# Kernel tuning notes

Hardware: AMD Instinct MI355X
Metric: run time of the kernel (lower is better)

Reference implementation:

```python
import jax, jax.numpy as jnp
import numpy as np
from jax import lax

H = 512      # hidden_dim
P = 11       # num_patches
T = 200      # patch_size
STRIDE = 180 # patch_stride
L = 2000     # output_length
C = 8        # num_target_channels
B = 1024


def _conv1d(x, w, b, pad):
    # x: (B, Cin, L), w: (Cout, Cin, K) torch OIH layout
    y = lax.conv_general_dilated(x, w, window_strides=(1,), padding=[(pad, pad)],
                                 dimension_numbers=('NCH', 'OIH', 'NCH'))
    return y + b[None, :, None]


def _window():
    fade = min(T // 4, 50)
    w = jnp.ones((T,), dtype=jnp.float32)
    ramp = jnp.linspace(0.0, 1.0, fade, dtype=jnp.float32)
    w = w.at[:fade].set(ramp)
    w = w.at[T - fade:].set(ramp[::-1])
    return w


def setup_inputs() -> dict:
    key = jax.random.key(0)
    ks = jax.random.split(key, 16)
    s = 0.02
    return {
        'expanded_embeddings': jax.random.normal(ks[0], (B, P, C, H), dtype=jnp.float32),
        # patch_decoder: Linear(H,H) -> GELU -> (Dropout eval=identity) -> Linear(H,T)
        'W1': jax.random.normal(ks[1], (H, H), dtype=jnp.float32) * s,
        'b1': jnp.zeros((H,), dtype=jnp.float32),
        'W2': jax.random.normal(ks[2], (H, T), dtype=jnp.float32) * s,
        'b2': jnp.zeros((T,), dtype=jnp.float32),
        # refinement: Conv1d(C,4C,15,p7) GELU Conv1d(4C,2C,15,p7) GELU Conv1d(2C,C,15,p7)
        'rw1': jax.random.normal(ks[3], (4 * C, C, 15), dtype=jnp.float32) * s,
        'rb1': jnp.zeros((4 * C,), dtype=jnp.float32),
        'rw2': jax.random.normal(ks[4], (2 * C, 4 * C, 15), dtype=jnp.float32) * s,
        'rb2': jnp.zeros((2 * C,), dtype=jnp.float32),
        'rw3': jax.random.normal(ks[5], (C, 2 * C, 15), dtype=jnp.float32) * s,
        'rb3': jnp.zeros((C,), dtype=jnp.float32),
        # output_proj: Conv1d(C,C,1)
        'pw': jax.random.normal(ks[6], (C, C, 1), dtype=jnp.float32) * s,
        'pb': jnp.zeros((C,), dtype=jnp.float32),
    }


def reference(expanded_embeddings, W1, b1, W2, b2, rw1, rb1, rw2, rb2, rw3, rb3, pw, pb):
    gelu = lambda x: jax.nn.gelu(x, approximate=False)  # torch default GELU (erf)
    # per-patch MLP decode: (B,P,C,H) -> (B,P,C,T)
    h = gelu(jnp.einsum('bpch,hd->bpcd', expanded_embeddings, W1) + b1)
    patches = jnp.einsum('bpch,ht->bpct', h, W2) + b2

    # overlap-add with triangular-faded window
    win = _window()  # (T,)
    out = jnp.zeros((B, C, L), dtype=jnp.float32)
    wsum = jnp.zeros((L,), dtype=jnp.float32)  # identical across B,C
    for i in range(P):  # small static loop over patches
        s0 = i * STRIDE
        if s0 + T <= L:
            out = out.at[:, :, s0:s0 + T].add(patches[:, i] * win)
            wsum = wsum.at[s0:s0 + T].add(win)
    rec = out / jnp.clip(wsum, 1e-8)[None, None, :]

    # conv refinement + residual
    r = gelu(_conv1d(rec, rw1, rb1, 7))
    r = gelu(_conv1d(r, rw2, rb2, 7))
    r = _conv1d(r, rw3, rb3, 7)
    rec = rec + r
    return _conv1d(rec, pw, pb, 0)
```

## Files before the change

### kernel.cpp

```cpp
#include <hip/hip_runtime.h>
#include <stdint.h>
#include <stddef.h>

#define HD 512
#define NP 11
#define PT 200
#define PSTRIDE 180
#define OL 2000
#define NC 8
#define NB 1024

typedef __bf16 bf16x8 __attribute__((ext_vector_type(8)));
typedef float floatx4 __attribute__((ext_vector_type(4)));
typedef unsigned short ushort8v __attribute__((ext_vector_type(8)));

__device__ __forceinline__ unsigned short f2bf(float f) {
    return __builtin_bit_cast(unsigned short, (__bf16)f);
}
__device__ __forceinline__ float bf2f(unsigned short s) {
    return __uint_as_float(((unsigned int)s) << 16);
}
__device__ __forceinline__ float gelu_erf(float x) {
    float z  = x * 0.70710678118654752440f;
    float az = __builtin_fabsf(z);
    float t  = __builtin_amdgcn_rcpf(__builtin_fmaf(0.3275911f, az, 1.0f));
    float p  = __builtin_fmaf(1.061405429f, t, -1.453152027f);
    p = __builtin_fmaf(p, t, 1.421413741f);
    p = __builtin_fmaf(p, t, -0.284496736f);
    p = __builtin_fmaf(p, t, 0.254829592f);
    p = p * t;
    float e    = __expf(-az * az);
    float erfa = __builtin_fmaf(-p, e, 1.0f);
    float erfz = (z < 0.0f) ? -erfa : erfa;
    return 0.5f * x * (1.0f + erfz);
}
__device__ __forceinline__ void async16(const unsigned short* g, unsigned short* l) {
    __builtin_amdgcn_global_load_lds(
        (const __attribute__((address_space(1))) unsigned int*)g,
        (__attribute__((address_space(3))) unsigned int*)l, 16, 0, 0);
}

__global__ __launch_bounds__(256) void prep_w_kernel(const float* __restrict__ W1,
                                                     const float* __restrict__ W2,
                                                     unsigned short* __restrict__ W1t,
                                                     unsigned short* __restrict__ W2t) {
    int idx = blockIdx.x * 256 + threadIdx.x;
    if (idx < 512 * 512) {
        int n = idx >> 9, k = idx & 511;
        W1t[idx] = f2bf(W1[k * 512 + n]);
    } else {
        int j = idx - 512 * 512;
        int n = j >> 9, k = j & 511;
        W2t[j] = (n < PT) ? f2bf(W2[k * PT + n]) : (unsigned short)0;
    }
}

__global__ __launch_bounds__(256) void prep_cw_kernel(const float* __restrict__ rw1,
                                                      const float* __restrict__ rw2,
                                                      const float* __restrict__ rw3,
                                                      unsigned short* __restrict__ Wt1,
                                                      unsigned short* __restrict__ Wt2,
                                                      unsigned short* __restrict__ Wt3) {
    int idx = blockIdx.x * 256 + threadIdx.x;
    if (idx < 4096) {
        int kb = idx >> 10, rem = idx & 1023, oc = rem >> 5, k = rem & 31;
        int tl = k >> 3, ic = k & 7, tap = kb * 4 + tl;
        Wt1[idx] = (tap < 15) ? f2bf(rw1[(oc * 8 + ic) * 15 + tap]) : (unsigned short)0;
    } else if (idx < 4096 + 7680) {
        int j = idx - 4096;
        int t = j >> 9, rem = j & 511, oc = rem >> 5, ic = rem & 31;
        Wt2[j] = f2bf(rw2[(oc * 32 + ic) * 15 + t]);
    } else {
        int j = idx - 11776;
        int kb = j >> 9, rem = j & 511, m = rem >> 5, k = rem & 31;
        int tl = k >> 4, ic = k & 15, tap = kb * 2 + tl;
        Wt3[j] = (m < 8 && tap < 15) ? f2bf(rw3[(m * 16 + ic) * 15 + tap]) : (unsigned short)0;
    }
}

template<bool A_FP32, bool FUSE_GELU, bool OUT_BF16, int LOG2_NT>
__global__ __launch_bounds__(256) void gemm_lds_kernel(const void* __restrict__ Ain,
                                                       const unsigned short* __restrict__ Bt,
                                                       const float* __restrict__ bias,
                                                       void* __restrict__ Cout,
                                                       int out_stride, int n_valid) {
    __shared__ __align__(16) unsigned short As[128 * 32];
    __shared__ __align__(16) unsigned short Bs[128 * 32];
    const float* Af          = (const float*)Ain;
    const unsigned short* Ab = (const unsigned short*)Ain;
    const int tid  = threadIdx.x;
    const int lane = tid & 63;
    const int wid  = tid >> 6;
    const int bid  = blockIdx.x;
    const int nt   = (bid >> 3) & ((1 << LOG2_NT) - 1);
    const int mt   = (bid >> (3 + LOG2_NT)) * 8 + (bid & 7);
    const int m0 = mt * 128;
    const int n0 = nt * 128;
    const int mw = (wid >> 1) * 64;
    const int nw = (wid & 1) * 64;
    const int l15  = lane & 15;
    const int quad = lane >> 4;
    const int srow = lane >> 2;
    const int scol = (lane & 3) * 8;

    floatx4 acc[4][4];
#pragma unroll
    for (int i = 0; i < 4; ++i)
#pragma unroll
        for (int j = 0; j < 4; ++j) acc[i][j] = (floatx4)0.0f;

    float4 pv[2][2];
    auto loadA = [&](int k0) {
#pragma unroll
        for (int p = 0; p < 2; ++p) {
            const float* g = Af + (size_t)(m0 + wid * 32 + p * 16 + srow) * 512 + k0 + scol;
            pv[p][0] = *(const float4*)g;
            pv[p][1] = *(const float4*)(g + 4);
        }
    };
    if (A_FP32) loadA(0);

    for (int k0 = 0; k0 < 512; k0 += 32) {
#pragma unroll
        for (int p = 0; p < 2; ++p) {
            const int rbase = wid * 32 + p * 16;
            if (A_FP32) {
                ushort8v o;
                o[0] = f2bf(pv[p][0].x); o[1] = f2bf(pv[p][0].y);
                o[2] = f2bf(pv[p][0].z); o[3] = f2bf(pv[p][0].w);
                o[4] = f2bf(pv[p][1].x); o[5] = f2bf(pv[p][1].y);
                o[6] = f2bf(pv[p][1].z); o[7] = f2bf(pv[p][1].w);
                *(ushort8v*)(As + (rbase + srow) * 32 + scol) = o;
            } else {
                async16(Ab + (size_t)(m0 + rbase + srow) * 512 + k0 + scol, As + rbase * 32);
            }
            async16(Bt + (size_t)(n0 + rbase + srow) * 512 + k0 + scol, Bs + rbase * 32);
        }
        __syncthreads();
        if (A_FP32 && k0 + 32 < 512) loadA(k0 + 32);
        bf16x8 af[4], bfr[4];
#pragma unroll
        for (int t = 0; t < 4; ++t) {
            af[t]  = *(const bf16x8*)(As + (mw + t * 16 + l15) * 32 + quad * 8);
            bfr[t] = *(const bf16x8*)(Bs + (nw + t * 16 + l15) * 32 + quad * 8);
        }
#pragma unroll
        for (int mtl = 0; mtl < 4; ++mtl)
#pragma unroll
            for (int ntl = 0; ntl < 4; ++ntl)
                acc[mtl][ntl] = __builtin_amdgcn_mfma_f32_16x16x32_bf16(af[mtl], bfr[ntl], acc[mtl][ntl], 0, 0, 0);
        __syncthreads();
    }

#pragma unroll
    for (int mtl = 0; mtl < 4; ++mtl) {
#pragma unroll
        for (int ntl = 0; ntl < 4; ++ntl) {
            const int col  = n0 + nw + ntl * 16 + l15;
            const int rowb = m0 + mw + mtl * 16 + quad * 4;
            const bool colok = (col < n_valid);
            float bv = colok ? bias[col] : 0.0f;
#pragma unroll
            for (int r = 0; r < 4; ++r) {
                float v = acc[mtl][ntl][r] + bv;
                if (FUSE_GELU) v = gelu_erf(v);
                if (colok) {
                    size_t off = (size_t)(rowb + r) * out_stride + col;
                    if (OUT_BF16) ((unsigned short*)Cout)[off] = f2bf(v);
                    else          ((float*)Cout)[off] = v;
                }
            }
        }
    }
}

__global__ __launch_bounds__(256) void tail_fused(const unsigned short* __restrict__ pat,
                                                  const unsigned short* __restrict__ Wt1,
                                                  const float* __restrict__ rb1,
                                                  const unsigned short* __restrict__ Wt2,
                                                  const float* __restrict__ rb2,
                                                  const unsigned short* __restrict__ Wt3,
                                                  const float* __restrict__ rb3,
                                                  const float* __restrict__ pw,
                                                  const float* __restrict__ pb,
                                                  float* __restrict__ out) {
    __shared__ __align__(16) unsigned short xs[304 * 8];
    __shared__ __align__(16) unsigned short ys1[288 * 40];
    __shared__ __align__(16) unsigned short ys2[272 * 24];
    __shared__ __align__(16) float r2[256 * 12];
    __shared__ float pws[64], bs1[32], bs2[16], bs3[8], bsp[8];
    const int tid = threadIdx.x;
    const int b = blockIdx.y;
    const int seg0 = blockIdx.x * 256;
    const int lane = tid & 63, wid = tid >> 6;
    const int l15 = lane & 15, quad = lane >> 4;

    if (tid < 64) pws[tid] = pw[tid];
    else if (tid < 96)  bs1[tid - 64]  = rb1[tid - 64];
    else if (tid < 112) bs2[tid - 96]  = rb2[tid - 96];
    else if (tid < 120) bs3[tid - 112] = rb3[tid - 112];
    else if (tid < 128) bsp[tid - 120] = pb[tid - 120];

    for (int row = tid; row < 304; row += 256) {
        int p = seg0 - 21 + row;
        float acc[8];
#pragma unroll
        for (int c = 0; c < 8; ++c) acc[c] = 0.0f;
        if (p >= 0 && p < OL) {
            int imin = (p >= PT) ? (p - (PT - PSTRIDE)) / PSTRIDE : 0;
            int imax = p / PSTRIDE; if (imax > NP - 1) imax = NP - 1;
            float wsum = 0.0f;
            for (int i = imin; i <= imax; ++i) {
                int t = p - i * PSTRIDE;
                float w = (t < 50) ? t * (1.0f / 49.0f)
                                   : ((t >= 150) ? (199 - t) * (1.0f / 49.0f) : 1.0f);
                wsum += w;
                const unsigned short* pp = pat + ((size_t)(b * NP + i) * NC) * PT + t;
#pragma unroll
                for (int c = 0; c < 8; ++c) acc[c] += bf2f(pp[c * PT]) * w;
            }
            float inv = 1.0f / fmaxf(wsum, 1e-8f);
#pragma unroll
            for (int c = 0; c < 8; ++c) acc[c] *= inv;
        }
        ushort4 o0, o1;
        o0.x = f2bf(acc[0]); o0.y = f2bf(acc[1]); o0.z = f2bf(acc[2]); o0.w = f2bf(acc[3]);
        o1.x = f2bf(acc[4]); o1.y = f2bf(acc[5]); o1.z = f2bf(acc[6]); o1.w = f2bf(acc[7]);
        *(ushort4*)(xs + row * 8)     = o0;
        *(ushort4*)(xs + row * 8 + 4) = o1;
        int cr = row - 21;
        if (cr >= 0 && cr < 256) {
            float4 v0 = { acc[0], acc[1], acc[2], acc[3] };
            float4 v1 = { acc[4], acc[5], acc[6], acc[7] };
            *(float4*)(r2 + cr * 12)     = v0;
            *(float4*)(r2 + cr * 12 + 4) = v1;
        }
    }
    __syncthreads();

    {
        bf16x8 wf[4][2];
#pragma unroll
        for (int kb = 0; kb < 4; ++kb)
#pragma unroll
            for (int ot = 0; ot < 2; ++ot)
                wf[kb][ot] = *(const bf16x8*)(Wt1 + (kb * 32 + ot * 16 + l15) * 32 + quad * 8);
#pragma unroll
        for (int u = 0; u < 5; ++u) {
            const int base = wid * 80 + u * 16;
            if (base < 288) {
                const int posl = base + l15;
                floatx4 a0 = (floatx4)0.0f, a1 = (floatx4)0.0f;
#pragma unroll
                for (int kb = 0; kb < 4; ++kb) {
                    int row = posl + kb * 4 + quad;
                    bf16x8 bfrag = *(const bf16x8*)(xs + row * 8);
                    a0 = __builtin_amdgcn_mfma_f32_16x16x32_bf16(wf[kb][0], bfrag, a0, 0, 0, 0);
                    a1 = __builtin_amdgcn_mfma_f32_16x16x32_bf16(wf[kb][1], bfrag, a1, 0, 0, 0);
                }
                int oc0 = quad * 4;
                ushort4 o;
                o.x = f2bf(gelu_erf(a0[0] + bs1[oc0]));
                o.y = f2bf(gelu_erf(a0[1] + bs1[oc0 + 1]));
                o.z = f2bf(gelu_erf(a0[2] + bs1[oc0 + 2]));
                o.w = f2bf(gelu_erf(a0[3] + bs1[oc0 + 3]));
                *(ushort4*)(ys1 + posl * 40 + oc0) = o;
                int oc1 = 16 + quad * 4;
                o.x = f2bf(gelu_erf(a1[0] + bs1[oc1]));
                o.y = f2bf(gelu_erf(a1[1] + bs1[oc1 + 1]));
                o.z = f2bf(gelu_erf(a1[2] + bs1[oc1 + 2]));
                o.w = f2bf(gelu_erf(a1[3] + bs1[oc1 + 3]));
                *(ushort4*)(ys1 + posl * 40 + oc1) = o;
            }
        }
    }
    __syncthreads();

    {
        bf16x8 wf[15];
#pragma unroll
        for (int t = 0; t < 15; ++t)
            wf[t] = *(const bf16x8*)(Wt2 + (t * 16 + l15) * 32 + quad * 8);
#pragma unroll
        for (int u = 0; u < 5; ++u) {
            const int base = wid * 80 + u * 16;
            if (base < 272) {
                const int posl = base + l15;
                floatx4 a = (floatx4)0.0f;
#pragma unroll
                for (int t = 0; t < 15; ++t) {
                    bf16x8 bfrag = *(const bf16x8*)(ys1 + (posl + t) * 40 + quad * 8);
                    a = __builtin_amdgcn_mfma_f32_16x16x32_bf16(wf[t], bfrag, a, 0, 0, 0);
                }
                int oc0 = quad * 4;
                ushort4 o;
                o.x = f2bf(gelu_erf(a[0] + bs2[oc0]));
                o.y = f2bf(gelu_erf(a[1] + bs2[oc0 + 1]));
                o.z = f2bf(gelu_erf(a[2] + bs2[oc0 + 2]));
                o.w = f2bf(gelu_erf(a[3] + bs2[oc0 + 3]));
                *(ushort4*)(ys2 + posl * 24 + oc0) = o;
            }
        }
    }
    __syncthreads();

    {
        bf16x8 wf[8];
#pragma unroll
        for (int kb = 0; kb < 8; ++kb)
            wf[kb] = *(const bf16x8*)(Wt3 + (kb * 16 + l15) * 32 + quad * 8);
#pragma unroll
        for (int u = 0; u < 5; ++u) {
            const int base = wid * 80 + u * 16;
            if (base < 256) {
                const int posl = base + l15;
                floatx4 a = (floatx4)0.0f;
#pragma unroll
                for (int kb = 0; kb < 8; ++kb) {
                    int row = posl + kb * 2 + (quad >> 1);
                    bf16x8 bfrag = *(const bf16x8*)(ys2 + row * 24 + (quad & 1) * 8);
                    a = __builtin_amdgcn_mfma_f32_16x16x32_bf16(wf[kb], bfrag, a, 0, 0, 0);
                }
                if (quad < 2) {
                    int oc0 = quad * 4;
                    float4 rv = *(const float4*)(r2 + posl * 12 + oc0);
                    rv.x += a[0] + bs3[oc0];
                    rv.y += a[1] + bs3[oc0 + 1];
                    rv.z += a[2] + bs3[oc0 + 2];
                    rv.w += a[3] + bs3[oc0 + 3];
                    *(float4*)(r2 + posl * 12 + oc0) = rv;
                }
            }
        }
    }
    __syncthreads();

    {
        int p = seg0 + tid;
        if (p < OL) {
            float4 a = *(const float4*)(r2 + tid * 12);
            float4 c = *(const float4*)(r2 + tid * 12 + 4);
#pragma unroll
            for (int o = 0; o < 8; ++o) {
                float v = bsp[o];
                v += pws[o * 8 + 0] * a.x + pws[o * 8 + 1] * a.y + pws[o * 8 + 2] * a.z + pws[o * 8 + 3] * a.w;
                v += pws[o * 8 + 4] * c.x + pws[o * 8 + 5] * c.y + pws[o * 8 + 6] * c.z + pws[o * 8 + 7] * c.w;
                out[((size_t)b * 8 + o) * OL + p] = v;
            }
        }
    }
}

extern "C" void kernel_launch(void* const* d_in, const int* in_sizes, int n_in,
                              void* d_out, int out_size, void* d_ws, size_t ws_size,
                              hipStream_t stream) {
    const float* X   = (const float*)d_in[0];
    const float* W1  = (const float*)d_in[1];
    const float* b1  = (const float*)d_in[2];
    const float* W2  = (const float*)d_in[3];
    const float* b2  = (const float*)d_in[4];
    const float* rw1 = (const float*)d_in[5];
    const float* rb1 = (const float*)d_in[6];
    const float* rw2 = (const float*)d_in[7];
    const float* rb2 = (const float*)d_in[8];
    const float* rw3 = (const float*)d_in[9];
    const float* rb3 = (const float*)d_in[10];
    const float* pw  = (const float*)d_in[11];
    const float* pb  = (const float*)d_in[12];
    float* out = (float*)d_out;

    char* ws = (char*)d_ws;
    unsigned short* W1t = (unsigned short*)(ws +  92274688);
    unsigned short* W2t = (unsigned short*)(ws +  92798976);
    unsigned short* h   = (unsigned short*)(ws +  93061120);
    unsigned short* pat = (unsigned short*)(ws + 185335808);
    unsigned short* Wt1 = (unsigned short*)(ws + 322961408);
    unsigned short* Wt2 = (unsigned short*)(ws + 322969600);
    unsigned short* Wt3 = (unsigned short*)(ws + 322984960);

    prep_w_kernel<<<1536, 256, 0, stream>>>(W1, W2, W1t, W2t);
    prep_cw_kernel<<<62, 256, 0, stream>>>(rw1, rw2, rw3, Wt1, Wt2, Wt3);
    gemm_lds_kernel<true,  true,  true, 2><<<2816, 256, 0, stream>>>((const void*)X, W1t, b1, (void*)h,   512, 512);
    gemm_lds_kernel<false, false, true, 1><<<1408, 256, 0, stream>>>((const void*)h,  W2t, b2, (void*)pat, 200, 200);
    tail_fused<<<dim3(8, NB), 256, 0, stream>>>(pat, Wt1, rb1, Wt2, rb2, Wt3, rb3, pw, pb, out);
}
```

Measured before the change: 548.1 us.

## Load GEMM MFMA fragments directly from global memory instead of staging through LDS

Both GEMM kernels drop the shared-memory tiles and barriers. Each wave now loads its A and B MFMA fragments straight from global memory into registers, with one-step register prefetch of the next k-slice. This removes LDS traffic and __syncthreads stalls. In exchange, tiles are no longer shared across the waves in a block: each A and B row is fetched by two waves, so L2/global traffic doubles and register pressure rises.

```diff
diff --git a/kernel.cpp b/kernel.cpp
--- a/kernel.cpp
+++ b/kernel.cpp
@@ -33,11 +33,6 @@
     float erfa = __builtin_fmaf(-p, e, 1.0f);
     float erfz = (z < 0.0f) ? -erfa : erfa;
     return 0.5f * x * (1.0f + erfz);
-}
-__device__ __forceinline__ void async16(const unsigned short* g, unsigned short* l) {
-    __builtin_amdgcn_global_load_lds(
-        (const __attribute__((address_space(1))) unsigned int*)g,
-        (__attribute__((address_space(3))) unsigned int*)l, 16, 0, 0);
 }
 
 __global__ __launch_bounds__(256) void prep_w_kernel(const float* __restrict__ W1,
@@ -79,13 +74,11 @@
 }
 
 template<bool A_FP32, bool FUSE_GELU, bool OUT_BF16, int LOG2_NT>
-__global__ __launch_bounds__(256) void gemm_lds_kernel(const void* __restrict__ Ain,
-                                                       const unsigned short* __restrict__ Bt,
-                                                       const float* __restrict__ bias,
-                                                       void* __restrict__ Cout,
-                                                       int out_stride, int n_valid) {
-    __shared__ __align__(16) unsigned short As[128 * 32];
-    __shared__ __align__(16) unsigned short Bs[128 * 32];
+__global__ __launch_bounds__(256) void gemm_direct_kernel(const void* __restrict__ Ain,
+                                                          const unsigned short* __restrict__ Bt,
+                                                          const float* __restrict__ bias,
+                                                          void* __restrict__ Cout,
+                                                          int out_stride, int n_valid) {
     const float* Af          = (const float*)Ain;
     const unsigned short* Ab = (const unsigned short*)Ain;
     const int tid  = threadIdx.x;
@@ -100,8 +93,9 @@
     const int nw = (wid & 1) * 64;
     const int l15  = lane & 15;
     const int quad = lane >> 4;
-    const int srow = lane >> 2;
-    const int scol = (lane & 3) * 8;
+
+    const size_t abase = (size_t)(m0 + mw + l15) * 512 + quad * 8;
+    const size_t bbase = (size_t)(n0 + nw + l15) * 512 + quad * 8;
 
     floatx4 acc[4][4];
 #pragma unroll
@@ -109,47 +103,58 @@
 #pragma unroll
         for (int j = 0; j < 4; ++j) acc[i][j] = (floatx4)0.0f;
 
-    float4 pv[2][2];
+    float4 fa[4][2];
+    bf16x8 nA[4];
+    bf16x8 nB[4];
+
+    auto loadB = [&](int k0) {
+#pragma unroll
+        for (int t = 0; t < 4; ++t)
+            nB[t] = *(const bf16x8*)(Bt + bbase + (size_t)t * 16 * 512 + k0);
+    };
     auto loadA = [&](int k0) {
-#pragma unroll
-        for (int p = 0; p < 2; ++p) {
-            const float* g = Af + (size_t)(m0 + wid * 32 + p * 16 + srow) * 512 + k0 + scol;
-            pv[p][0] = *(const float4*)g;
-            pv[p][1] = *(const float4*)(g + 4);
+        if (A_FP32) {
+#pragma unroll
+            for (int t = 0; t < 4; ++t) {
+                const float* g = Af + abase + (size_t)t * 16 * 512 + k0;
+                fa[t][0] = *(const float4*)g;
+                fa[t][1] = *(const float4*)(g + 4);
+            }
+        } else {
+#pragma unroll
+            for (int t = 0; t < 4; ++t)
+                nA[t] = *(const bf16x8*)(Ab + abase + (size_t)t * 16 * 512 + k0);
         }
     };
-    if (A_FP32) loadA(0);
-
-    for (int k0 = 0; k0 < 512; k0 += 32) {
-#pragma unroll
-        for (int p = 0; p < 2; ++p) {
-            const int rbase = wid * 32 + p * 16;
-            if (A_FP32) {
+
+    loadA(0);
+    loadB(0);
+
+    for (int it = 0; it < 16; ++it) {
+        const int kn = it * 32 + 32;
+        bf16x8 af[4], bfr[4];
+        if (A_FP32) {
+#pragma unroll
+            for (int t = 0; t < 4; ++t) {
                 ushort8v o;
-                o[0] = f2bf(pv[p][0].x); o[1] = f2bf(pv[p][0].y);
-                o[2] = f2bf(pv[p][0].z); o[3] = f2bf(pv[p][0].w);
-                o[4] = f2bf(pv[p][1].x); o[5] = f2bf(pv[p][1].y);
-                o[6] = f2bf(pv[p][1].z); o[7] = f2bf(pv[p][1].w);
-                *(ushort8v*)(As + (rbase + srow) * 32 + scol) = o;
-            } else {
-                async16(Ab + (size_t)(m0 + rbase + srow) * 512 + k0 + scol, As + rbase * 32);
-            }
-            async16(Bt + (size_t)(n0 + rbase + srow) * 512 + k0 + scol, Bs + rbase * 32);
-        }
-        __syncthreads();
-        if (A_FP32 && k0 + 32 < 512) loadA(k0 + 32);
-        bf16x8 af[4], bfr[4];
-#pragma unroll
-        for (int t = 0; t < 4; ++t) {
-            af[t]  = *(const bf16x8*)(As + (mw + t * 16 + l15) * 32 + quad * 8);
-            bfr[t] = *(const bf16x8*)(Bs + (nw + t * 16 + l15) * 32 + quad * 8);
-        }
+                o[0] = f2bf(fa[t][0].x); o[1] = f2bf(fa[t][0].y);
+                o[2] = f2bf(fa[t][0].z); o[3] = f2bf(fa[t][0].w);
+                o[4] = f2bf(fa[t][1].x); o[5] = f2bf(fa[t][1].y);
+                o[6] = f2bf(fa[t][1].z); o[7] = f2bf(fa[t][1].w);
+                af[t] = __builtin_bit_cast(bf16x8, o);
+            }
+        } else {
+#pragma unroll
+            for (int t = 0; t < 4; ++t) af[t] = nA[t];
+        }
+#pragma unroll
+        for (int t = 0; t < 4; ++t) bfr[t] = nB[t];
+        if (kn < 512) { loadA(kn); loadB(kn); }
 #pragma unroll
         for (int mtl = 0; mtl < 4; ++mtl)
 #pragma unroll
             for (int ntl = 0; ntl < 4; ++ntl)
                 acc[mtl][ntl] = __builtin_amdgcn_mfma_f32_16x16x32_bf16(af[mtl], bfr[ntl], acc[mtl][ntl], 0, 0, 0);
-        __syncthreads();
     }
 
 #pragma unroll
@@ -380,7 +385,7 @@
 
     prep_w_kernel<<<1536, 256, 0, stream>>>(W1, W2, W1t, W2t);
     prep_cw_kernel<<<62, 256, 0, stream>>>(rw1, rw2, rw3, Wt1, Wt2, Wt3);
-    gemm_lds_kernel<true,  true,  true, 2><<<2816, 256, 0, stream>>>((const void*)X, W1t, b1, (void*)h,   512, 512);
-    gemm_lds_kernel<false, false, true, 1><<<1408, 256, 0, stream>>>((const void*)h,  W2t, b2, (void*)pat, 200, 200);
+    gemm_direct_kernel<true,  true,  true, 2><<<2816, 256, 0, stream>>>((const void*)X, W1t, b1, (void*)h,   512, 512);
+    gemm_direct_kernel<false, false, true, 1><<<1408, 256, 0, stream>>>((const void*)h,  W2t, b2, (void*)pat, 200, 200);
     tail_fused<<<dim3(8, NB), 256, 0, stream>>>(pat, Wt1, rb1, Wt2, rb2, Wt3, rb3, pw, pb, out);
 }
```

Result: slower. 737.0 us (+34.5%).
